# Performance work log

Measured on AMD Instinct MI355X. Metric: run time of the kernel, lower is better.

## Reference

```python
import jax, jax.numpy as jnp
import numpy as np

NL, BS, NQ, D, NH, HD, L, P, DFF, NC = 6, 16, 300, 256, 8, 32, 3, 4, 1024, 80
SHAPES = np.array([[80, 80], [40, 40], [20, 20]], np.int32)  # (H, W) per level: 640x640 input, strides 8/16/32
STARTS = np.array([0, 6400, 8000], np.int32)
LV = 8400  # sum H*W


def setup_inputs():
    keys = iter(jax.random.split(jax.random.key(0), 64))

    def rn(shape, s=0.02):
        return jax.random.normal(next(keys), shape, jnp.float32) * s

    return {
        "tgt": rn((BS, NQ, D), 1.0),
        "ref_points_unact": rn((BS, NQ, 4), 1.0),
        "memory": rn((BS, LV, D), 1.0),
        "spatial_shapes": jnp.asarray(SHAPES),
        "level_start_index": jnp.asarray(STARTS),
        "Wq": rn((NL, D, D)), "bq": rn((NL, D)),
        "Wk": rn((NL, D, D)), "bk": rn((NL, D)),
        "Wv": rn((NL, D, D)), "bv": rn((NL, D)),
        "Wo": rn((NL, D, D)), "bo": rn((NL, D)),
        "ln1_g": jnp.ones((NL, D)), "ln1_b": jnp.zeros((NL, D)),
        "ln2_g": jnp.ones((NL, D)), "ln2_b": jnp.zeros((NL, D)),
        "ln3_g": jnp.ones((NL, D)), "ln3_b": jnp.zeros((NL, D)),
        "Wvp": rn((NL, D, D)), "bvp": rn((NL, D)),
        "Woff": rn((NL, D, NH * L * P * 2)), "boff": rn((NL, NH * L * P * 2), 0.5),
        "Waw": rn((NL, D, NH * L * P)), "baw": rn((NL, NH * L * P)),
        "Wop": rn((NL, D, D)), "bop": rn((NL, D)),
        "Wff1": rn((NL, D, DFF)), "bff1": rn((NL, DFF)),
        "Wff2": rn((NL, DFF, D)), "bff2": rn((NL, D)),
        "Wb1": rn((NL, D, D)), "bb1": rn((NL, D)),
        "Wb2": rn((NL, D, D)), "bb2": rn((NL, D)),
        "Wb3": rn((NL, D, 4)), "bb3": rn((NL, 4)),
        "Ws": rn((NL, D, NC)), "bs_": rn((NL, NC)),
        "Wp1": rn((4, 2 * D)), "bp1": rn((2 * D,)),
        "Wp2": rn((2 * D, D)), "bp2": rn((D,)),
    }


def _ln(x, g, b):
    m = x.mean(-1, keepdims=True)
    v = ((x - m) ** 2).mean(-1, keepdims=True)
    return (x - m) * jax.lax.rsqrt(v + 1e-5) * g + b


def _inv_sigmoid(x, eps=1e-5):
    x = jnp.clip(x, 0.0, 1.0)
    return jnp.log(jnp.clip(x, eps, None)) - jnp.log(jnp.clip(1.0 - x, eps, None))


def _forward(shapes, starts, tgt, ref_points_unact, memory, Wq, bq, Wk, bk, Wv, bv, Wo, bo, ln1_g, ln1_b, ln2_g, ln2_b, ln3_g, ln3_b, Wvp, bvp, Woff, boff, Waw, baw, Wop, bop, Wff1, bff1, Wff2, bff2, Wb1, bb1, Wb2, bb2, Wb3, bb3, Ws, bs_, Wp1, bp1, Wp2, bp2):
    bs, Lq, _ = tgt.shape

    def mha(q, k, v, i):
        qh = (q @ Wq[i] + bq[i]).reshape(bs, Lq, NH, HD)
        kh = (k @ Wk[i] + bk[i]).reshape(bs, Lq, NH, HD)
        vh = (v @ Wv[i] + bv[i]).reshape(bs, Lq, NH, HD)
        att = jax.nn.softmax(jnp.einsum('bqhd,bkhd->bhqk', qh, kh) / np.float32(np.sqrt(HD)), -1)
        return jnp.einsum('bhqk,bkhd->bqhd', att, vh).reshape(bs, Lq, D) @ Wo[i] + bo[i]

    def deform(query, ref, i):
        # multi-scale deformable attention (Deformable-DETR core, bilinear, zero padding)
        val = (memory @ Wvp[i] + bvp[i]).reshape(bs, -1, NH, HD).transpose(0, 2, 1, 3)  # [bs,NH,Lv,HD]
        off = (query @ Woff[i] + boff[i]).reshape(bs, Lq, NH, L, P, 2)
        aw = jax.nn.softmax((query @ Waw[i] + baw[i]).reshape(bs, Lq, NH, L * P), -1).reshape(bs, Lq, NH, L, P)
        r = ref[:, :, None, None, None, :]  # [bs,Lq,1,1,1,4] box (cx,cy,w,h)
        loc = r[..., :2] + off / P * r[..., 2:] * 0.5  # [bs,Lq,NH,L,P,2]
        out = jnp.zeros((bs, NH, Lq, HD), query.dtype)
        for lvl in range(L):
            H, W = int(shapes[lvl, 0]), int(shapes[lvl, 1])
            s = int(starts[lvl])
            vl = val[:, :, s:s + H * W]  # [bs,NH,H*W,HD]
            x = loc[:, :, :, lvl, :, 0].transpose(0, 2, 1, 3) * W - 0.5  # [bs,NH,Lq,P] (align_corners=False)
            y = loc[:, :, :, lvl, :, 1].transpose(0, 2, 1, 3) * H - 0.5
            x0 = jnp.floor(x).astype(jnp.int32)
            y0 = jnp.floor(y).astype(jnp.int32)
            wx, wy = x - x0, y - y0

            def g(xi, yi):
                valid = ((xi >= 0) & (xi < W) & (yi >= 0) & (yi < H)).astype(query.dtype)
                idx = jnp.clip(yi, 0, H - 1) * W + jnp.clip(xi, 0, W - 1)
                gat = jnp.take_along_axis(vl, idx.reshape(bs, NH, Lq * P, 1), axis=2)
                return gat.reshape(bs, NH, Lq, P, HD) * valid[..., None]

            samp = (g(x0, y0) * ((1 - wx) * (1 - wy))[..., None]
                    + g(x0 + 1, y0) * (wx * (1 - wy))[..., None]
                    + g(x0, y0 + 1) * ((1 - wx) * wy)[..., None]
                    + g(x0 + 1, y0 + 1) * (wx * wy)[..., None])
            awl = aw[:, :, :, lvl].transpose(0, 2, 1, 3)  # [bs,NH,Lq,P]
            out = out + (samp * awl[..., None]).sum(3)
        return out.transpose(0, 2, 1, 3).reshape(bs, Lq, D) @ Wop[i] + bop[i]

    ref_d = jax.nn.sigmoid(ref_points_unact)
    out = tgt
    bboxes = logits = None
    for i in range(NL):
        qpos = jax.nn.relu(ref_d @ Wp1 + bp1) @ Wp2 + bp2  # query_pos_head MLP(4 -> 512 -> 256)
        q = out + qpos
        out = _ln(out + mha(q, q, out, i), ln1_g[i], ln1_b[i])
        out = _ln(out + deform(out + qpos, ref_d, i), ln2_g[i], ln2_b[i])
        out = _ln(out + jax.nn.relu(out @ Wff1[i] + bff1[i]) @ Wff2[i] + bff2[i], ln3_g[i], ln3_b[i])
        h = jax.nn.relu(out @ Wb1[i] + bb1[i])
        h = jax.nn.relu(h @ Wb2[i] + bb2[i])
        inter = jax.nn.sigmoid(h @ Wb3[i] + bb3[i] + _inv_sigmoid(ref_d))
        if i == NL - 1:  # eval_idx = -1 -> outputs taken at last layer (inference path)
            bboxes = inter[None]
            logits = (out @ Ws[i] + bs_[i])[None]
        ref_d = inter
    return bboxes, logits


def reference(tgt, ref_points_unact, memory, spatial_shapes, level_start_index, Wq, bq, Wk, bk, Wv, bv, Wo, bo, ln1_g, ln1_b, ln2_g, ln2_b, ln3_g, ln3_b, Wvp, bvp, Woff, boff, Waw, baw, Wop, bop, Wff1, bff1, Wff2, bff2, Wb1, bb1, Wb2, bb2, Wb3, bb3, Ws, bs_, Wp1, bp1, Wp2, bp2):
    shapes = np.asarray(spatial_shapes)
    starts = np.asarray(level_start_index)
    return _forward(shapes, starts, tgt, ref_points_unact, memory, Wq, bq, Wk, bk, Wv, bv, Wo, bo, ln1_g, ln1_b, ln2_g, ln2_b, ln3_g, ln3_b, Wvp, bvp, Woff, boff, Waw, baw, Wop, bop, Wff1, bff1, Wff2, bff2, Wb1, bb1, Wb2, bb2, Wb3, bb3, Ws, bs_, Wp1, bp1, Wp2, bp2)
```

## Files before the change

kernel.cpp:

```cpp
#include <hip/hip_runtime.h>

#define NLAYERS 6
#define BSZ 16
#define NQL 300
#define DM 256
#define NHEAD 8
#define HDIM 32
#define NLVL 3
#define NPT 4
#define DFFN 1024
#define NCLS 80
#define LVTOT 8400
#define NROW (BSZ * NQL)
#define MEMN (BSZ * LVTOT)

typedef __attribute__((ext_vector_type(8))) short bf16x8;
typedef __attribute__((ext_vector_type(8))) ushort us8;
typedef __attribute__((ext_vector_type(4))) float f32x4;

__device__ __forceinline__ float b2f(ushort u) {
    return __uint_as_float(((uint)u) << 16);
}
__device__ __forceinline__ ushort f2b(float f) {
    uint i = __float_as_uint(f);
    uint r = i + 0x7fffu + ((i >> 16) & 1u);
    return (ushort)(r >> 16);
}
__device__ __forceinline__ void split2(float v, ushort& h, ushort& l) {
    ushort hh = f2b(v);
    h = hh;
    l = f2b(v - b2f(hh));
}
__device__ __forceinline__ void gl_lds16(const void* g, void* l) {
    __builtin_amdgcn_global_load_lds(
        (const __attribute__((address_space(1))) unsigned int*)g,
        (__attribute__((address_space(3))) unsigned int*)l, 16, 0, 0);
}

__global__ __launch_bounds__(256) void f2b_kernel(
    const float* __restrict__ src, ushort* __restrict__ dst, int n)
{
    int i = (blockIdx.x * 256 + threadIdx.x) * 4;
    if (i < n) {
        float4 v = *(const float4*)&src[i];
        ushort4 o = {f2b(v.x), f2b(v.y), f2b(v.z), f2b(v.w)};
        *(ushort4*)&dst[i] = o;
    }
}

__global__ __launch_bounds__(256) void split_kernel(
    const float* __restrict__ src, ushort* __restrict__ dh,
    ushort* __restrict__ dl, int n)
{
    int i = (blockIdx.x * 256 + threadIdx.x) * 4;
    if (i < n) {
        float4 v = *(const float4*)&src[i];
        ushort4 h, l;
        split2(v.x, h.x, l.x);
        split2(v.y, h.y, l.y);
        split2(v.z, h.z, l.z);
        split2(v.w, h.w, l.w);
        *(ushort4*)&dh[i] = h;
        *(ushort4*)&dl[i] = l;
    }
}

#define NTE 14
struct TTab {
    const float* s[NTE];
    ushort* d[NTE];
    int K[NTE], N[NTE], dls[NTE], dr0[NTE];
    int tstart[NTE + 1];
};

__global__ __launch_bounds__(256) void transpose_batch_kernel(TTab tab)
{
    __shared__ float tile[32][33];
    const int bx = blockIdx.x;
    int e = 0;
    while (e < NTE - 1 && bx >= tab.tstart[e + 1]) ++e;
    const int local = bx - tab.tstart[e];
    const int K = tab.K[e], N = tab.N[e];
    const int tx_n = (N + 31) >> 5, ty_n = (K + 31) >> 5;
    const int perB = tx_n * ty_n;
    const int z = local / perB;
    const int rem = local - z * perB;
    const int tyi = rem / tx_n, txi = rem - tyi * tx_n;
    const float* src = tab.s[e] + (size_t)z * K * N;
    ushort* dh = tab.d[e] + (size_t)z * tab.dls[e] + (size_t)tab.dr0[e] * K;
    const int n0 = txi * 32, k0 = tyi * 32;
    const int tx = threadIdx.x, ty = threadIdx.y;
    for (int r = 0; r < 32; r += 8) {
        int k = k0 + ty + r, n = n0 + tx;
        if (k < K && n < N) tile[ty + r][tx] = src[(size_t)k * N + n];
    }
    __syncthreads();
    for (int r = 0; r < 32; r += 8) {
        int n = n0 + ty + r, k = k0 + tx;
        if (n < N && k < K) dh[(size_t)n * K + k] = f2b(tile[tx][ty + r]);
    }
}

__global__ __launch_bounds__(256) void concat2_kernel(
    const float* __restrict__ a, int na, const float* __restrict__ b, int nb,
    float* __restrict__ dst, int nl)
{
    const int tot = na + nb;
    int i = blockIdx.x * 256 + threadIdx.x;
    if (i < nl * tot) {
        int l = i / tot, j = i - l * tot;
        dst[i] = (j < na) ? a[l * na + j] : b[l * nb + j - na];
    }
}

template <int ACT>
__global__ __launch_bounds__(256) void gemm_ps(
    const ushort* __restrict__ Ahp, const ushort* __restrict__ Alp,
    const ushort* __restrict__ BTh, const float* __restrict__ bias,
    int M, int N, int K,
    float* __restrict__ Cf, const float* __restrict__ addsrc,
    ushort* __restrict__ Ch, ushort* __restrict__ Cl)
{
    __shared__ __align__(16) ushort Ahs[2][64 * 32];
    __shared__ __align__(16) ushort Als[2][64 * 32];
    __shared__ __align__(16) ushort Bhs[2][64 * 32];

    const int tid  = threadIdx.x;
    const int m0   = blockIdx.x * 64;
    const int n0   = blockIdx.y * 64;
    const int wv   = tid >> 6;
    const int lane = tid & 63;
    const int lm   = lane & 15;
    const int lq   = lane >> 4;
    const int r    = tid >> 2;
    const int c8   = (tid & 3) * 8;

    gl_lds16(&Ahp[(size_t)(m0 + r) * K + c8], &Ahs[0][r * 32 + c8]);
    gl_lds16(&Alp[(size_t)(m0 + r) * K + c8], &Als[0][r * 32 + c8]);
    gl_lds16(&BTh[(size_t)(n0 + r) * K + c8], &Bhs[0][r * 32 + c8]);
    __syncthreads();

    f32x4 acc[4] = {};
    int buf = 0;
    for (int k0 = 32; k0 < K + 32; k0 += 32) {
        const int nxt = buf ^ 1;
        if (k0 < K) {
            gl_lds16(&Ahp[(size_t)(m0 + r) * K + k0 + c8], &Ahs[nxt][r * 32 + c8]);
            gl_lds16(&Alp[(size_t)(m0 + r) * K + k0 + c8], &Als[nxt][r * 32 + c8]);
            gl_lds16(&BTh[(size_t)(n0 + r) * K + k0 + c8], &Bhs[nxt][r * 32 + c8]);
        }
        bf16x8 afh = *(const bf16x8*)&Ahs[buf][(wv * 16 + lm) * 32 + lq * 8];
        bf16x8 afl = *(const bf16x8*)&Als[buf][(wv * 16 + lm) * 32 + lq * 8];
#pragma unroll
        for (int nb = 0; nb < 4; ++nb) {
            bf16x8 bfh = *(const bf16x8*)&Bhs[buf][(nb * 16 + lm) * 32 + lq * 8];
            acc[nb] = __builtin_amdgcn_mfma_f32_16x16x32_bf16(afh, bfh, acc[nb], 0, 0, 0);
            acc[nb] = __builtin_amdgcn_mfma_f32_16x16x32_bf16(afl, bfh, acc[nb], 0, 0, 0);
        }
        __syncthreads();
        buf = nxt;
    }

    const int row = m0 + wv * 16 + lq * 4;
#pragma unroll
    for (int nb = 0; nb < 4; ++nb) {
        int col = n0 + nb * 16 + lm;
        if (col < N) {
            float bv = bias ? bias[col] : 0.f;
#pragma unroll
            for (int rr = 0; rr < 4; ++rr) {
                float v = acc[nb][rr] + bv;
                if (ACT) v = fmaxf(v, 0.f);
                const size_t idx = (size_t)(row + rr) * N + col;
                if (Cf) Cf[idx] = v;
                if (Ch) {
                    float w = addsrc ? (v + addsrc[idx]) : v;
                    ushort h, l;
                    split2(w, h, l);
                    Ch[idx] = h;
                    if (Cl) Cl[idx] = l;
                }
            }
        }
    }
}

__global__ __launch_bounds__(256) void gemm_qkv(
    const ushort* __restrict__ qhp, const ushort* __restrict__ qlp,
    const ushort* __restrict__ ohp, const ushort* __restrict__ olp,
    const ushort* __restrict__ Bqk, const ushort* __restrict__ Bv,
    const float* __restrict__ biasqk, const float* __restrict__ biasv,
    ushort* __restrict__ Cqk, ushort* __restrict__ Cv)
{
    constexpr int K = 256;
    __shared__ __align__(16) ushort Ahs[2][64 * 32];
    __shared__ __align__(16) ushort Als[2][64 * 32];
    __shared__ __align__(16) ushort Bhs[2][64 * 32];

    const int by = blockIdx.y;
    const ushort *Ahp, *Alp, *BTh;
    const float* bias;
    ushort* Ch;
    int N, n0;
    if (by < 8) { Ahp = qhp; Alp = qlp; BTh = Bqk; bias = biasqk; Ch = Cqk; N = 512; n0 = by * 64; }
    else        { Ahp = ohp; Alp = olp; BTh = Bv;  bias = biasv;  Ch = Cv;  N = 256; n0 = (by - 8) * 64; }

    const int tid  = threadIdx.x;
    const int m0   = blockIdx.x * 64;
    const int wv   = tid >> 6;
    const int lane = tid & 63;
    const int lm   = lane & 15;
    const int lq   = lane >> 4;
    const int r    = tid >> 2;
    const int c8   = (tid & 3) * 8;

    gl_lds16(&Ahp[(size_t)(m0 + r) * K + c8], &Ahs[0][r * 32 + c8]);
    gl_lds16(&Alp[(size_t)(m0 + r) * K + c8], &Als[0][r * 32 + c8]);
    gl_lds16(&BTh[(size_t)(n0 + r) * K + c8], &Bhs[0][r * 32 + c8]);
    __syncthreads();

    f32x4 acc[4] = {};
    int buf = 0;
    for (int k0 = 32; k0 < K + 32; k0 += 32) {
        const int nxt = buf ^ 1;
        if (k0 < K) {
            gl_lds16(&Ahp[(size_t)(m0 + r) * K + k0 + c8], &Ahs[nxt][r * 32 + c8]);
            gl_lds16(&Alp[(size_t)(m0 + r) * K + k0 + c8], &Als[nxt][r * 32 + c8]);
            gl_lds16(&BTh[(size_t)(n0 + r) * K + k0 + c8], &Bhs[nxt][r * 32 + c8]);
        }
        bf16x8 afh = *(const bf16x8*)&Ahs[buf][(wv * 16 + lm) * 32 + lq * 8];
        bf16x8 afl = *(const bf16x8*)&Als[buf][(wv * 16 + lm) * 32 + lq * 8];
#pragma unroll
        for (int nb = 0; nb < 4; ++nb) {
            bf16x8 bfh = *(const bf16x8*)&Bhs[buf][(nb * 16 + lm) * 32 + lq * 8];
            acc[nb] = __builtin_amdgcn_mfma_f32_16x16x32_bf16(afh, bfh, acc[nb], 0, 0, 0);
            acc[nb] = __builtin_amdgcn_mfma_f32_16x16x32_bf16(afl, bfh, acc[nb], 0, 0, 0);
        }
        __syncthreads();
        buf = nxt;
    }

    const int row = m0 + wv * 16 + lq * 4;
#pragma unroll
    for (int nb = 0; nb < 4; ++nb) {
        const int col = n0 + nb * 16 + lm;
        const float bv = bias[col];
#pragma unroll
        for (int rr = 0; rr < 4; ++rr)
            Ch[(size_t)(row + rr) * N + col] = f2b(acc[nb][rr] + bv);
    }
}

__global__ __launch_bounds__(256) void gemm_big(
    const ushort* __restrict__ Abf, const ushort* __restrict__ BTh,
    const float* __restrict__ bias, ushort* __restrict__ C,
    int M, int N, int K)
{
    __shared__ __align__(16) ushort As[128 * 32];
    __shared__ __align__(16) ushort Bs[128 * 32];
    const int tid = threadIdx.x;
    const int n0 = blockIdx.x * 128, m0 = blockIdx.y * 128;
    const int wv = tid >> 6, lane = tid & 63;
    const int lm = lane & 15, quad = lane >> 4;
    const int wr = wv >> 1, wc = wv & 1;
    const int srow = lane >> 2;
    const int scol = (lane & 3) * 8;

    f32x4 acc[4][4] = {};

    for (int k0 = 0; k0 < K; k0 += 32) {
        __syncthreads();
#pragma unroll
        for (int s2 = 0; s2 < 2; ++s2) {
            const int seg = wv * 2 + s2;
            const int row = seg * 16 + srow;
            gl_lds16(&Abf[(size_t)(m0 + row) * K + k0 + scol],
                     &As[seg * 512 + lane * 8]);
            gl_lds16(&BTh[(size_t)(n0 + row) * K + k0 + scol],
                     &Bs[seg * 512 + lane * 8]);
        }
        __syncthreads();

        bf16x8 af[4], bfr[4];
#pragma unroll
        for (int i = 0; i < 4; ++i)
            af[i] = *(const bf16x8*)&As[(wr * 64 + i * 16 + lm) * 32 + quad * 8];
#pragma unroll
        for (int i = 0; i < 4; ++i)
            bfr[i] = *(const bf16x8*)&Bs[(wc * 64 + i * 16 + lm) * 32 + quad * 8];
#pragma unroll
        for (int mi = 0; mi < 4; ++mi)
#pragma unroll
            for (int ni = 0; ni < 4; ++ni)
                acc[mi][ni] = __builtin_amdgcn_mfma_f32_16x16x32_bf16(
                    af[mi], bfr[ni], acc[mi][ni], 0, 0, 0);
    }

#pragma unroll
    for (int ni = 0; ni < 4; ++ni) {
        const int col = n0 + wc * 64 + ni * 16 + lm;
        const float bv = bias[col];
#pragma unroll
        for (int mi = 0; mi < 4; ++mi) {
            const int row = m0 + wr * 64 + mi * 16 + quad * 4;
#pragma unroll
            for (int rr = 0; rr < 4; ++rr)
                C[(size_t)(row + rr) * N + col] = f2b(acc[mi][ni][rr] + bv);
        }
    }
}

__global__ __launch_bounds__(256) void mha_mfma_kernel(
    const ushort* __restrict__ qh, int ldq, const ushort* __restrict__ kh, int ldk,
    const ushort* __restrict__ vh, int ldv,
    ushort* __restrict__ outh, ushort* __restrict__ outl)
{
    __shared__ ushort Kh[304 * 36];
    __shared__ ushort Vth[32 * 328];
    __shared__ ushort Pb[4][16 * 168];

    const int tid = threadIdx.x;
    const int wv = tid >> 6, lane = tid & 63;
    const int bh = blockIdx.x >> 1, half = blockIdx.x & 1;
    const int b = bh >> 3, h = bh & 7;
    const size_t qbase = (size_t)b * NQL * ldq + h * HDIM;
    const size_t kbase = (size_t)b * NQL * ldk + h * HDIM;
    const size_t vbase = (size_t)b * NQL * ldv + h * HDIM;
    const size_t obase = (size_t)b * NQL * DM + h * HDIM;

    for (int idx = tid; idx < 304 * 32; idx += 256) {
        int row = idx >> 5, d = idx & 31;
        Kh[row * 36 + d] = (row < NQL) ? kh[kbase + (size_t)row * ldk + d] : (ushort)0;
    }
    for (int idx = tid; idx < 328 * 32; idx += 256) {
        int key = idx >> 5, d = idx & 31;
        Vth[d * 328 + key] = (key < NQL) ? vh[vbase + (size_t)key * ldv + d] : (ushort)0;
    }
    for (int i = lane; i < 16 * 168; i += 64) Pb[wv][i] = 0;
    __syncthreads();

    const int quad = lane >> 4, c = lane & 15;
    const float scale = 0.17677669529663687f;

    const int qt_beg = (half ? 10 : 0) + wv;
    const int qt_end = (half ? 19 : 10);
    for (int qt = qt_beg; qt < qt_end; qt += 4) {
        const int q = qt * 16 + c;
        bf16x8 qf = *(const bf16x8*)&qh[qbase + (size_t)q * ldq + quad * 8];

        f32x4 sc[19];
#pragma unroll
        for (int kt = 0; kt < 19; ++kt) {
            bf16x8 kf = *(const bf16x8*)&Kh[(kt * 16 + c) * 36 + quad * 8];
            f32x4 a = {};
            a = __builtin_amdgcn_mfma_f32_16x16x32_bf16(qf, kf, a, 0, 0, 0);
            sc[kt] = a;
        }
        float inv4[4];
#pragma unroll
        for (int r = 0; r < 4; ++r) {
            float mx = -1e30f;
#pragma unroll
            for (int kt = 0; kt < 19; ++kt) {
                float s = sc[kt][r] * scale;
                if (kt * 16 + c >= NQL) s = -1e30f;
                sc[kt][r] = s;
                mx = fmaxf(mx, s);
            }
#pragma unroll
            for (int m = 1; m < 16; m <<= 1) mx = fmaxf(mx, __shfl_xor(mx, m, 64));
            float l = 0.f;
#pragma unroll
            for (int kt = 0; kt < 19; ++kt) {
                float p = __expf(sc[kt][r] - mx);
                sc[kt][r] = p;
                l += p;
            }
#pragma unroll
            for (int m = 1; m < 16; m <<= 1) l += __shfl_xor(l, m, 64);
            inv4[r] = 1.f / l;
        }

        f32x4 o0 = {}, o1 = {};
#pragma unroll
        for (int r = 0; r < 4; ++r)
#pragma unroll
            for (int kt = 0; kt < 10; ++kt)
                Pb[wv][(quad * 4 + r) * 168 + kt * 16 + c] = f2b(sc[kt][r] * inv4[r]);
#pragma unroll
        for (int ks = 0; ks < 5; ++ks) {
            bf16x8 pf = *(const bf16x8*)&Pb[wv][c * 168 + ks * 32 + quad * 8];
            bf16x8 v0 = *(const bf16x8*)&Vth[c * 328 + ks * 32 + quad * 8];
            bf16x8 v1 = *(const bf16x8*)&Vth[(16 + c) * 328 + ks * 32 + quad * 8];
            o0 = __builtin_amdgcn_mfma_f32_16x16x32_bf16(pf, v0, o0, 0, 0, 0);
            o1 = __builtin_amdgcn_mfma_f32_16x16x32_bf16(pf, v1, o1, 0, 0, 0);
        }
#pragma unroll
        for (int r = 0; r < 4; ++r) {
#pragma unroll
            for (int kt = 10; kt < 19; ++kt)
                Pb[wv][(quad * 4 + r) * 168 + (kt - 10) * 16 + c] = f2b(sc[kt][r] * inv4[r]);
            Pb[wv][(quad * 4 + r) * 168 + 144 + c] = 0;
        }
#pragma unroll
        for (int ks = 0; ks < 5; ++ks) {
            bf16x8 pf = *(const bf16x8*)&Pb[wv][c * 168 + ks * 32 + quad * 8];
            bf16x8 v0 = *(const bf16x8*)&Vth[c * 328 + 160 + ks * 32 + quad * 8];
            bf16x8 v1 = *(const bf16x8*)&Vth[(16 + c) * 328 + 160 + ks * 32 + quad * 8];
            o0 = __builtin_amdgcn_mfma_f32_16x16x32_bf16(pf, v0, o0, 0, 0, 0);
            o1 = __builtin_amdgcn_mfma_f32_16x16x32_bf16(pf, v1, o1, 0, 0, 0);
        }
#pragma unroll
        for (int r = 0; r < 4; ++r) {
            const int qq = qt * 16 + quad * 4 + r;
            if (qq < NQL) {
                ushort hh, ll;
                split2(o0[r], hh, ll);
                outh[obase + (size_t)qq * DM + c] = hh;
                outl[obase + (size_t)qq * DM + c] = ll;
                split2(o1[r], hh, ll);
                outh[obase + (size_t)qq * DM + 16 + c] = hh;
                outl[obase + (size_t)qq * DM + 16 + c] = ll;
            }
        }
    }
}

__global__ __launch_bounds__(256) void deform_kernel(
    const ushort* __restrict__ val, const float* __restrict__ offaw,
    const float* __restrict__ refd,
    ushort* __restrict__ samph, ushort* __restrict__ sampl)
{
    __shared__ float offs[192];
    __shared__ float aws[96];
    __shared__ float rr[4];
    const int row = blockIdx.x;
    const int b = row / NQL;
    const int t = threadIdx.x;
    if (t < 192) offs[t] = offaw[(size_t)row * 288 + t];
    if (t < 96)  aws[t] = offaw[(size_t)row * 288 + 192 + t];
    if (t < 4)   rr[t] = refd[row * 4 + t];
    __syncthreads();

    const int h = t >> 5, d = t & 31;
    float mx = -1e30f;
#pragma unroll
    for (int j = 0; j < 12; ++j) mx = fmaxf(mx, aws[h * 12 + j]);
    float ev[12]; float se = 0.f;
#pragma unroll
    for (int j = 0; j < 12; ++j) { ev[j] = __expf(aws[h * 12 + j] - mx); se += ev[j]; }
    const float inv = 1.f / se;

    const int HWs[3] = {80, 40, 20};
    const int STs[3] = {0, 6400, 8000};
    float acc = 0.f;
#pragma unroll
    for (int l = 0; l < NLVL; ++l) {
        const int Wd = HWs[l], Hd = HWs[l], st = STs[l];
#pragma unroll
        for (int p = 0; p < NPT; ++p) {
            const float w12 = ev[l * 4 + p] * inv;
            const float ox = offs[((h * 3 + l) * 4 + p) * 2 + 0];
            const float oy = offs[((h * 3 + l) * 4 + p) * 2 + 1];
            const float x = (rr[0] + ox * 0.125f * rr[2]) * Wd - 0.5f;
            const float y = (rr[1] + oy * 0.125f * rr[3]) * Hd - 0.5f;
            const float xf = floorf(x), yf = floorf(y);
            const int x0 = (int)xf, y0 = (int)yf;
            const float wx = x - xf, wy = y - yf;
            const float tw[4] = {(1 - wx) * (1 - wy), wx * (1 - wy),
                                 (1 - wx) * wy,       wx * wy};
            const int xs[4] = {x0, x0 + 1, x0, x0 + 1};
            const int ys[4] = {y0, y0, y0 + 1, y0 + 1};
            float sv = 0.f;
#pragma unroll
            for (int tp = 0; tp < 4; ++tp) {
                const int xi = xs[tp], yi = ys[tp];
                if (xi >= 0 && xi < Wd && yi >= 0 && yi < Hd) {
                    const int idx = st + yi * Wd + xi;
                    sv += tw[tp] * b2f(val[((size_t)b * LVTOT + idx) * DM + h * HDIM + d]);
                }
            }
            acc += w12 * sv;
        }
    }
    ushort hh, ll;
    split2(acc, hh, ll);
    samph[(size_t)row * DM + t] = hh;
    sampl[(size_t)row * DM + t] = ll;
}

__global__ __launch_bounds__(256) void addln_kernel(
    const float* x, const float* __restrict__ dl,
    const float* __restrict__ g, const float* __restrict__ bb,
    float* outf, ushort* __restrict__ outh, ushort* __restrict__ outl,
    const float* __restrict__ qpos, ushort* __restrict__ q2h, ushort* __restrict__ q2l)
{
    const int wv = threadIdx.x >> 6, lane = threadIdx.x & 63;
    const int row = blockIdx.x * 4 + wv;
    const size_t base = (size_t)row * DM + lane * 4;
    const float4 xv = *(const float4*)(x + base);
    const float4 dv = *(const float4*)(dl + base);
    float v[4] = {xv.x + dv.x, xv.y + dv.y, xv.z + dv.z, xv.w + dv.w};

    float s = v[0] + v[1] + v[2] + v[3];
#pragma unroll
    for (int m = 32; m; m >>= 1) s += __shfl_xor(s, m, 64);
    const float mean = s * (1.f / 256.f);
    float sq = 0.f;
#pragma unroll
    for (int j = 0; j < 4; ++j) { float dd = v[j] - mean; sq += dd * dd; }
#pragma unroll
    for (int m = 32; m; m >>= 1) sq += __shfl_xor(sq, m, 64);
    const float rstd = rsqrtf(sq * (1.f / 256.f) + 1e-5f);

    float y[4];
    ushort4 yh, yl;
#pragma unroll
    for (int j = 0; j < 4; ++j) {
        const int col = lane * 4 + j;
        y[j] = (v[j] - mean) * rstd * g[col] + bb[col];
    }
    *(float4*)(outf + base) = make_float4(y[0], y[1], y[2], y[3]);
    split2(y[0], yh.x, yl.x);
    split2(y[1], yh.y, yl.y);
    split2(y[2], yh.z, yl.z);
    split2(y[3], yh.w, yl.w);
    *(ushort4*)(outh + base) = yh;
    *(ushort4*)(outl + base) = yl;
    if (q2h) {
        const float4 qp = *(const float4*)(qpos + base);
        float q2v[4] = {y[0] + qp.x, y[1] + qp.y, y[2] + qp.z, y[3] + qp.w};
        ushort4 qh_, ql_;
        split2(q2v[0], qh_.x, ql_.x);
        split2(q2v[1], qh_.y, ql_.y);
        split2(q2v[2], qh_.z, ql_.z);
        split2(q2v[3], qh_.w, ql_.w);
        *(ushort4*)(q2h + base) = qh_;
        *(ushort4*)(q2l + base) = ql_;
    }
}

__global__ __launch_bounds__(256) void bbox_fused(
    const ushort* __restrict__ h2h, const ushort* __restrict__ h2l,
    const float* __restrict__ Wb3, const float* __restrict__ bb3,
    const float* __restrict__ rpu, float* __restrict__ refd,
    float* __restrict__ dout, int mode, int writeout,
    const float* __restrict__ Wp1, const float* __restrict__ bp1,
    ushort* __restrict__ t1h, ushort* __restrict__ t1l, int computeT1)
{
    __shared__ float hls[64 * 258];
    __shared__ float wb3s[1024];
    __shared__ float wp1s[4 * 512];
    __shared__ float bp1s[512];
    __shared__ float ref4[64 * 4];

    const int tid = threadIdx.x;
    const int r0 = blockIdx.x * 64;

    if (computeT1) {
        for (int i = tid; i < 2048; i += 256) wp1s[i] = Wp1[i];
        if (tid < 256) { bp1s[tid] = bp1[tid]; bp1s[tid + 256] = bp1[tid + 256]; }
    }
    if (mode == 1) {
        for (int i = tid; i < 1024; i += 256) wb3s[i] = Wb3[i];
        for (int j = tid; j < 2048; j += 256) {
            const int row = j >> 5, seg = (j & 31) * 8;
            const size_t g = (size_t)(r0 + row) * 256 + seg;
            us8 hv = *(const us8*)&h2h[g];
            us8 lv = *(const us8*)&h2l[g];
            float* o = &hls[row * 258 + seg];
#pragma unroll
            for (int x = 0; x < 8; ++x) o[x] = b2f(hv[x]) + b2f(lv[x]);
        }
    }
    __syncthreads();

    const int r = tid >> 2, c = tid & 3;
    float v;
    if (mode == 1) {
        float acc = 0.f;
        const float* hrow = &hls[r * 258];
#pragma unroll 4
        for (int k = 0; k < 256; ++k)
            acc = fmaf(hrow[k], wb3s[k * 4 + c], acc);
        const float b3v = acc + bb3[c];
        const float old = refd[(size_t)(r0 + r) * 4 + c];
        const float rc = fminf(fmaxf(old, 0.f), 1.f);
        const float invs = logf(fmaxf(rc, 1e-5f)) - logf(fmaxf(1.f - rc, 1e-5f));
        v = 1.f / (1.f + __expf(-(b3v + invs)));
    } else {
        v = 1.f / (1.f + __expf(-rpu[(size_t)(r0 + r) * 4 + c]));
    }
    refd[(size_t)(r0 + r) * 4 + c] = v;
    if (writeout) dout[(size_t)(r0 + r) * 4 + c] = v;
    ref4[r * 4 + c] = v;
    __syncthreads();

    if (!computeT1) return;
    for (int j = 0; j < 128; ++j) {
        const int idx = j * 256 + tid;
        const int row = idx >> 9, n = idx & 511;
        const float a0 = ref4[row * 4 + 0], a1 = ref4[row * 4 + 1];
        const float a2 = ref4[row * 4 + 2], a3 = ref4[row * 4 + 3];
        float t = bp1s[n];
        t = fmaf(a0, wp1s[n], t);
        t = fmaf(a1, wp1s[512 + n], t);
        t = fmaf(a2, wp1s[1024 + n], t);
        t = fmaf(a3, wp1s[1536 + n], t);
        t = fmaxf(t, 0.f);
        ushort hh, ll;
        split2(t, hh, ll);
        const size_t gg = (size_t)(r0 + row) * 512 + n;
        t1h[gg] = hh;
        t1l[gg] = ll;
    }
}

extern "C" void kernel_launch(void* const* d_in, const int* in_sizes, int n_in,
                              void* d_out, int out_size, void* d_ws, size_t ws_size,
                              hipStream_t stream)
{
    const float* tgt    = (const float*)d_in[0];
    const float* rpu    = (const float*)d_in[1];
    const float* memory = (const float*)d_in[2];
    const float* Wq  = (const float*)d_in[5];  const float* bq  = (const float*)d_in[6];
    const float* Wk  = (const float*)d_in[7];  const float* bk  = (const float*)d_in[8];
    const float* Wv  = (const float*)d_in[9];  const float* bv  = (const float*)d_in[10];
    const float* Wo  = (const float*)d_in[11]; const float* bo  = (const float*)d_in[12];
    const float* ln1g = (const float*)d_in[13]; const float* ln1b = (const float*)d_in[14];
    const float* ln2g = (const float*)d_in[15]; const float* ln2b = (const float*)d_in[16];
    const float* ln3g = (const float*)d_in[17]; const float* ln3b = (const float*)d_in[18];
    const float* Wvp = (const float*)d_in[19]; const float* bvp = (const float*)d_in[20];
    const float* Woff = (const float*)d_in[21]; const float* boff = (const float*)d_in[22];
    const float* Waw = (const float*)d_in[23]; const float* baw = (const float*)d_in[24];
    const float* Wop = (const float*)d_in[25]; const float* bop = (const float*)d_in[26];
    const float* Wff1 = (const float*)d_in[27]; const float* bff1 = (const float*)d_in[28];
    const float* Wff2 = (const float*)d_in[29]; const float* bff2 = (const float*)d_in[30];
    const float* Wb1 = (const float*)d_in[31]; const float* bb1 = (const float*)d_in[32];
    const float* Wb2 = (const float*)d_in[33]; const float* bb2 = (const float*)d_in[34];
    const float* Wb3 = (const float*)d_in[35]; const float* bb3 = (const float*)d_in[36];
    const float* Ws  = (const float*)d_in[37]; const float* bs_ = (const float*)d_in[38];
    const float* Wp1 = (const float*)d_in[39]; const float* bp1 = (const float*)d_in[40];
    const float* Wp2 = (const float*)d_in[41]; const float* bp2 = (const float*)d_in[42];

    size_t off = 0;
    auto alloc = [&](size_t elems, size_t elsz) -> void* {
        void* r = (char*)d_ws + off;
        off += elems * elsz;
        off = (off + 255) & ~(size_t)255;
        return r;
    };
    ushort *wqkh = (ushort*)alloc(6 * 131072, 2);
    ushort *wvh  = (ushort*)alloc(6 * 65536, 2);
    ushort *woh  = (ushort*)alloc(6 * 65536, 2);
    ushort *wvph = (ushort*)alloc(6 * 65536, 2);
    ushort *wfah = (ushort*)alloc(6 * 81920, 2);
    ushort *woph = (ushort*)alloc(6 * 65536, 2);
    ushort *wf1h = (ushort*)alloc(6 * 262144, 2);
    ushort *wf2h = (ushort*)alloc(6 * 262144, 2);
    ushort *wb1h = (ushort*)alloc(6 * 65536, 2);
    ushort *wb2h = (ushort*)alloc(6 * 65536, 2);
    ushort *wsh  = (ushort*)alloc(6 * 20480, 2);
    ushort *wp2h = (ushort*)alloc(131072, 2);
    float  *bqk  = (float*)alloc(6 * 512, 4);
    float  *bfa  = (float*)alloc(6 * 288, 4);

    ushort* mem_bf = (ushort*)alloc((size_t)MEMN * DM, 2);
    ushort* val_bf = (ushort*)alloc((size_t)MEMN * DM, 2);
    float*  out_f  = (float*)alloc(NROW * DM, 4);
    float*  qpos_f = (float*)alloc(NROW * DM, 4);
    float*  tmp_f  = (float*)alloc(NROW * DM, 4);
    float*  refd_f = (float*)alloc(NROW * 4, 4);
    float*  offaw_f = (float*)alloc(NROW * 288, 4);

    ushort* out_h = (ushort*)alloc(NROW * DM, 2);
    ushort* out_l = (ushort*)alloc(NROW * DM, 2);

    const size_t NN = NROW;
    ushort* scratch = (ushort*)alloc(NN * 2056, 2);
    ushort* q_h  = scratch;
    ushort* q_l  = scratch + NN * 256;
    ushort* vh_h = scratch + NN * 512;
    ushort* att_h = scratch;
    ushort* att_l = scratch + NN * 256;
    ushort* q2_h = scratch + NN * 512;
    ushort* q2_l = scratch + NN * 768;
    ushort* samp_h = scratch;
    ushort* samp_l = scratch + NN * 256;
    ushort* ff_h = scratch;
    ushort* ff_l = scratch + NN * 1024;
    ushort* h1_h = scratch;
    ushort* h1_l = scratch + NN * 256;
    ushort* h2_h = scratch + NN * 512;
    ushort* h2_l = scratch + NN * 768;
    ushort* t1_h = scratch + NN * 1024;
    ushort* t1_l = scratch + NN * 1536;
    ushort* qk_h = scratch + NN * 1024;

    if (off > ws_size) return;

    {
        TTab tab;
        const float* ss[NTE] = {Wq, Wk, Wv, Wo, Wvp, Woff, Waw, Wop,
                                Wff1, Wff2, Wb1, Wb2, Ws, Wp2};
        ushort* dd[NTE] = {wqkh, wqkh, wvh, woh, wvph, wfah, wfah, woph,
                           wf1h, wf2h, wb1h, wb2h, wsh, wp2h};
        const int KK[NTE]  = {256, 256, 256, 256, 256, 256, 256, 256,
                              256, 1024, 256, 256, 256, 512};
        const int NNe[NTE] = {256, 256, 256, 256, 256, 192, 96, 256,
                              1024, 256, 256, 256, 80, 256};
        const int BB[NTE]  = {6, 6, 6, 6, 6, 6, 6, 6, 6, 6, 6, 6, 6, 1};
        const int DL[NTE]  = {131072, 131072, 65536, 65536, 65536, 81920, 81920,
                              65536, 262144, 262144, 65536, 65536, 20480, 131072};
        const int DR[NTE]  = {0, 256, 0, 0, 0, 0, 192, 0, 0, 0, 0, 0, 0, 0};
        int total = 0;
        for (int e = 0; e < NTE; ++e) {
            tab.s[e] = ss[e]; tab.d[e] = dd[e];
            tab.K[e] = KK[e]; tab.N[e] = NNe[e];
            tab.dls[e] = DL[e]; tab.dr0[e] = DR[e];
            tab.tstart[e] = total;
            total += ((NNe[e] + 31) / 32) * ((KK[e] + 31) / 32) * BB[e];
        }
        tab.tstart[NTE] = total;
        transpose_batch_kernel<<<total, dim3(32, 8), 0, stream>>>(tab);
    }
    concat2_kernel<<<12, 256, 0, stream>>>(bq, 256, bk, 256, bqk, 6);
    concat2_kernel<<<7, 256, 0, stream>>>(boff, 192, baw, 96, bfa, 6);
    f2b_kernel<<<(MEMN * DM) / 1024, 256, 0, stream>>>(memory, mem_bf, MEMN * DM);

    hipMemcpyAsync(out_f, tgt, (size_t)NROW * DM * 4, hipMemcpyDeviceToDevice, stream);
    split_kernel<<<(NROW * DM) / 1024, 256, 0, stream>>>(tgt, out_h, out_l, NROW * DM);
    bbox_fused<<<75, 256, 0, stream>>>(nullptr, nullptr, Wb3, bb3, rpu, refd_f,
                                       nullptr, 0, 0, Wp1, bp1, t1_h, t1_l, 1);

    auto GP = [&](const ushort* Ahp, const ushort* Alp, const ushort* BTh,
                  const float* bias, int N, int K, bool relu,
                  float* Cf, ushort* Ch = nullptr, ushort* Cl = nullptr,
                  const float* addsrc = nullptr) {
        dim3 g(NROW / 64, (N + 63) / 64);
        if (relu) gemm_ps<1><<<g, 256, 0, stream>>>(Ahp, Alp, BTh, bias, NROW, N, K,
                                                    Cf, addsrc, Ch, Cl);
        else      gemm_ps<0><<<g, 256, 0, stream>>>(Ahp, Alp, BTh, bias, NROW, N, K,
                                                    Cf, addsrc, Ch, Cl);
    };

    for (int i = 0; i < NLAYERS; ++i) {
        GP(t1_h, t1_l, wp2h, bp2, 256, 512, false, qpos_f, q_h, q_l, out_f);
        gemm_qkv<<<dim3(NROW / 64, 12), 256, 0, stream>>>(
            q_h, q_l, out_h, out_l, wqkh + i * 131072, wvh + i * 65536,
            bqk + i * 512, bv + i * 256, qk_h, vh_h);
        mha_mfma_kernel<<<256, 256, 0, stream>>>(qk_h, 512, qk_h + 256, 512,
                                                 vh_h, 256, att_h, att_l);
        GP(att_h, att_l, woh + i * 65536, bo + i * 256, 256, 256, false, tmp_f);
        addln_kernel<<<1200, 256, 0, stream>>>(out_f, tmp_f, ln1g + i * 256, ln1b + i * 256,
                                               out_f, out_h, out_l, qpos_f, q2_h, q2_l);
        {
            dim3 g(DM / 128, MEMN / 128);
            gemm_big<<<g, 256, 0, stream>>>(mem_bf, wvph + i * 65536, bvp + i * 256,
                                            val_bf, MEMN, DM, DM);
        }
        GP(q2_h, q2_l, wfah + i * 81920, bfa + i * 288, 288, 256, false, offaw_f);
        deform_kernel<<<4800, 256, 0, stream>>>(val_bf, offaw_f, refd_f, samp_h, samp_l);
        GP(samp_h, samp_l, woph + i * 65536, bop + i * 256, 256, 256, false, tmp_f);
        addln_kernel<<<1200, 256, 0, stream>>>(out_f, tmp_f, ln2g + i * 256, ln2b + i * 256,
                                               out_f, out_h, out_l, nullptr, nullptr, nullptr);
        GP(out_h, out_l, wf1h + i * 262144, bff1 + i * 1024, 1024, 256, true,
           nullptr, ff_h, ff_l);
        GP(ff_h, ff_l, wf2h + i * 262144, bff2 + i * 256, 256, 1024, false, tmp_f);
        addln_kernel<<<1200, 256, 0, stream>>>(out_f, tmp_f, ln3g + i * 256, ln3b + i * 256,
                                               out_f, out_h, out_l, nullptr, nullptr, nullptr);
        GP(out_h, out_l, wb1h + i * 65536, bb1 + i * 256, 256, 256, true,
           nullptr, h1_h, h1_l);
        GP(h1_h, h1_l, wb2h + i * 65536, bb2 + i * 256, 256, 256, true,
           nullptr, h2_h, h2_l);
        const int last = (i == NLAYERS - 1);
        bbox_fused<<<75, 256, 0, stream>>>(h2_h, h2_l, Wb3 + i * 1024, bb3 + i * 4,
                                           nullptr, refd_f, (float*)d_out, 1,
                                           last ? 1 : 0, Wp1, bp1, t1_h, t1_l,
                                           last ? 0 : 1);
        if (last) {
            GP(out_h, out_l, wsh + i * 20480, bs_ + i * 80, 80, 256, false,
               (float*)d_out + NROW * 4);
        }
    }
}
```

Before: 2.105 ms.

## Split value-projection GEMM into chunks co-scheduled with small layer GEMMs

Removes the standalone memory value-projection GEMM and splits its 2100 tiles into three 700-tile chunks. Each chunk runs as extra blocks inside a combined kernel alongside one of the small per-layer GEMMs (query-pos, output projection, offset/attention-weight projection). The aim is to fill the GPU's idle compute units during the under-occupied small GEMMs and to cut launches. It also merges the two bias-concat kernels into one and vectorizes the t1 stores in bbox_fused to 8-wide writes. The cost is a larger LDS footprint for the small-GEMM blocks and more complex kernels.

Result: no change. 2.097 ms (-0.4%).

```diff
diff --git a/kernel.cpp b/kernel.cpp
--- a/kernel.cpp
+++ b/kernel.cpp
@@ -101,15 +101,23 @@
     }
 }
 
-__global__ __launch_bounds__(256) void concat2_kernel(
-    const float* __restrict__ a, int na, const float* __restrict__ b, int nb,
-    float* __restrict__ dst, int nl)
-{
-    const int tot = na + nb;
-    int i = blockIdx.x * 256 + threadIdx.x;
-    if (i < nl * tot) {
-        int l = i / tot, j = i - l * tot;
-        dst[i] = (j < na) ? a[l * na + j] : b[l * nb + j - na];
+__global__ __launch_bounds__(256) void concat_both_kernel(
+    const float* __restrict__ bq, const float* __restrict__ bk, float* __restrict__ bqk,
+    const float* __restrict__ boff, const float* __restrict__ baw, float* __restrict__ bfa)
+{
+    const int bx = blockIdx.x;
+    if (bx < 12) {
+        int i = bx * 256 + threadIdx.x;
+        if (i < 6 * 512) {
+            int l = i / 512, j = i - l * 512;
+            bqk[i] = (j < 256) ? bq[l * 256 + j] : bk[l * 256 + j - 256];
+        }
+    } else {
+        int i = (bx - 12) * 256 + threadIdx.x;
+        if (i < 6 * 288) {
+            int l = i / 288, j = i - l * 288;
+            bfa[i] = (j < 192) ? boff[l * 192 + j] : baw[l * 96 + j - 192];
+        }
     }
 }
 
@@ -185,6 +193,137 @@
     }
 }
 
+__global__ __launch_bounds__(256) void gemm_mix(
+    const ushort* __restrict__ Ahp, const ushort* __restrict__ Alp,
+    const ushort* __restrict__ BTh, const float* __restrict__ bias,
+    int N, int K,
+    float* __restrict__ Cf, const float* __restrict__ addsrc,
+    ushort* __restrict__ Ch, ushort* __restrict__ Cl,
+    int nSmall,
+    const ushort* __restrict__ gA, const ushort* __restrict__ gB,
+    const float* __restrict__ gbias, ushort* __restrict__ gC,
+    int chunkOff)
+{
+    __shared__ __align__(16) ushort lds[12288];
+
+    const int tid  = threadIdx.x;
+    const int wv   = tid >> 6;
+    const int lane = tid & 63;
+    const int lm   = lane & 15;
+    const int lq   = lane >> 4;
+
+    if ((int)blockIdx.x < nSmall) {
+        typedef ushort (*lds2)[64 * 32];
+        lds2 Ahs = (lds2)lds;
+        lds2 Als = (lds2)(lds + 4096);
+        lds2 Bhs = (lds2)(lds + 8192);
+        const int m0 = (blockIdx.x % 75) * 64;
+        const int n0 = (blockIdx.x / 75) * 64;
+        const int r  = tid >> 2;
+        const int c8 = (tid & 3) * 8;
+
+        gl_lds16(&Ahp[(size_t)(m0 + r) * K + c8], &Ahs[0][r * 32 + c8]);
+        gl_lds16(&Alp[(size_t)(m0 + r) * K + c8], &Als[0][r * 32 + c8]);
+        gl_lds16(&BTh[(size_t)(n0 + r) * K + c8], &Bhs[0][r * 32 + c8]);
+        __syncthreads();
+
+        f32x4 acc[4] = {};
+        int buf = 0;
+        for (int k0 = 32; k0 < K + 32; k0 += 32) {
+            const int nxt = buf ^ 1;
+            if (k0 < K) {
+                gl_lds16(&Ahp[(size_t)(m0 + r) * K + k0 + c8], &Ahs[nxt][r * 32 + c8]);
+                gl_lds16(&Alp[(size_t)(m0 + r) * K + k0 + c8], &Als[nxt][r * 32 + c8]);
+                gl_lds16(&BTh[(size_t)(n0 + r) * K + k0 + c8], &Bhs[nxt][r * 32 + c8]);
+            }
+            bf16x8 afh = *(const bf16x8*)&Ahs[buf][(wv * 16 + lm) * 32 + lq * 8];
+            bf16x8 afl = *(const bf16x8*)&Als[buf][(wv * 16 + lm) * 32 + lq * 8];
+#pragma unroll
+            for (int nb = 0; nb < 4; ++nb) {
+                bf16x8 bfh = *(const bf16x8*)&Bhs[buf][(nb * 16 + lm) * 32 + lq * 8];
+                acc[nb] = __builtin_amdgcn_mfma_f32_16x16x32_bf16(afh, bfh, acc[nb], 0, 0, 0);
+                acc[nb] = __builtin_amdgcn_mfma_f32_16x16x32_bf16(afl, bfh, acc[nb], 0, 0, 0);
+            }
+            __syncthreads();
+            buf = nxt;
+        }
+
+        const int row = m0 + wv * 16 + lq * 4;
+#pragma unroll
+        for (int nb = 0; nb < 4; ++nb) {
+            int col = n0 + nb * 16 + lm;
+            if (col < N) {
+                float bv = bias[col];
+#pragma unroll
+                for (int rr = 0; rr < 4; ++rr) {
+                    float v = acc[nb][rr] + bv;
+                    const size_t idx = (size_t)(row + rr) * N + col;
+                    if (Cf) Cf[idx] = v;
+                    if (Ch) {
+                        float w = addsrc ? (v + addsrc[idx]) : v;
+                        ushort h, l;
+                        split2(w, h, l);
+                        Ch[idx] = h;
+                        if (Cl) Cl[idx] = l;
+                    }
+                }
+            }
+        }
+    } else {
+        ushort* As = lds;
+        ushort* Bs = lds + 4096;
+        const int bid = (int)blockIdx.x - nSmall + chunkOff;
+        const int n0 = (bid & 1) * 128;
+        const int m0 = (bid >> 1) * 128;
+        const int wr = wv >> 1, wc = wv & 1;
+        const int srow = lane >> 2;
+        const int scol = (lane & 3) * 8;
+
+        f32x4 acc[4][4] = {};
+
+        for (int k0 = 0; k0 < 256; k0 += 32) {
+            __syncthreads();
+#pragma unroll
+            for (int s2 = 0; s2 < 2; ++s2) {
+                const int seg = wv * 2 + s2;
+                const int row = seg * 16 + srow;
+                gl_lds16(&gA[(size_t)(m0 + row) * 256 + k0 + scol],
+                         &As[seg * 512 + lane * 8]);
+                gl_lds16(&gB[(size_t)(n0 + row) * 256 + k0 + scol],
+                         &Bs[seg * 512 + lane * 8]);
+            }
+            __syncthreads();
+
+            bf16x8 af[4], bfr[4];
+#pragma unroll
+            for (int i = 0; i < 4; ++i)
+                af[i] = *(const bf16x8*)&As[(wr * 64 + i * 16 + lm) * 32 + lq * 8];
+#pragma unroll
+            for (int i = 0; i < 4; ++i)
+                bfr[i] = *(const bf16x8*)&Bs[(wc * 64 + i * 16 + lm) * 32 + lq * 8];
+#pragma unroll
+            for (int mi = 0; mi < 4; ++mi)
+#pragma unroll
+                for (int ni = 0; ni < 4; ++ni)
+                    acc[mi][ni] = __builtin_amdgcn_mfma_f32_16x16x32_bf16(
+                        af[mi], bfr[ni], acc[mi][ni], 0, 0, 0);
+        }
+
+#pragma unroll
+        for (int ni = 0; ni < 4; ++ni) {
+            const int col = n0 + wc * 64 + ni * 16 + lm;
+            const float bv = gbias[col];
+#pragma unroll
+            for (int mi = 0; mi < 4; ++mi) {
+                const int row = m0 + wr * 64 + mi * 16 + lq * 4;
+#pragma unroll
+                for (int rr = 0; rr < 4; ++rr)
+                    gC[(size_t)(row + rr) * 256 + col] = f2b(acc[mi][ni][rr] + bv);
+            }
+        }
+    }
+}
+
 __global__ __launch_bounds__(256) void gemm_qkv(
     const ushort* __restrict__ qhp, const ushort* __restrict__ qlp,
     const ushort* __restrict__ ohp, const ushort* __restrict__ olp,
@@ -248,65 +387,6 @@
 #pragma unroll
         for (int rr = 0; rr < 4; ++rr)
             Ch[(size_t)(row + rr) * N + col] = f2b(acc[nb][rr] + bv);
-    }
-}
-
-__global__ __launch_bounds__(256) void gemm_big(
-    const ushort* __restrict__ Abf, const ushort* __restrict__ BTh,
-    const float* __restrict__ bias, ushort* __restrict__ C,
-    int M, int N, int K)
-{
-    __shared__ __align__(16) ushort As[128 * 32];
-    __shared__ __align__(16) ushort Bs[128 * 32];
-    const int tid = threadIdx.x;
-    const int n0 = blockIdx.x * 128, m0 = blockIdx.y * 128;
-    const int wv = tid >> 6, lane = tid & 63;
-    const int lm = lane & 15, quad = lane >> 4;
-    const int wr = wv >> 1, wc = wv & 1;
-    const int srow = lane >> 2;
-    const int scol = (lane & 3) * 8;
-
-    f32x4 acc[4][4] = {};
-
-    for (int k0 = 0; k0 < K; k0 += 32) {
-        __syncthreads();
-#pragma unroll
-        for (int s2 = 0; s2 < 2; ++s2) {
-            const int seg = wv * 2 + s2;
-            const int row = seg * 16 + srow;
-            gl_lds16(&Abf[(size_t)(m0 + row) * K + k0 + scol],
-                     &As[seg * 512 + lane * 8]);
-            gl_lds16(&BTh[(size_t)(n0 + row) * K + k0 + scol],
-                     &Bs[seg * 512 + lane * 8]);
-        }
-        __syncthreads();
-
-        bf16x8 af[4], bfr[4];
-#pragma unroll
-        for (int i = 0; i < 4; ++i)
-            af[i] = *(const bf16x8*)&As[(wr * 64 + i * 16 + lm) * 32 + quad * 8];
-#pragma unroll
-        for (int i = 0; i < 4; ++i)
-            bfr[i] = *(const bf16x8*)&Bs[(wc * 64 + i * 16 + lm) * 32 + quad * 8];
-#pragma unroll
-        for (int mi = 0; mi < 4; ++mi)
-#pragma unroll
-            for (int ni = 0; ni < 4; ++ni)
-                acc[mi][ni] = __builtin_amdgcn_mfma_f32_16x16x32_bf16(
-                    af[mi], bfr[ni], acc[mi][ni], 0, 0, 0);
-    }
-
-#pragma unroll
-    for (int ni = 0; ni < 4; ++ni) {
-        const int col = n0 + wc * 64 + ni * 16 + lm;
-        const float bv = bias[col];
-#pragma unroll
-        for (int mi = 0; mi < 4; ++mi) {
-            const int row = m0 + wr * 64 + mi * 16 + quad * 4;
-#pragma unroll
-            for (int rr = 0; rr < 4; ++rr)
-                C[(size_t)(row + rr) * N + col] = f2b(acc[mi][ni][rr] + bv);
-        }
     }
 }
 
@@ -597,22 +677,29 @@
     __syncthreads();
 
     if (!computeT1) return;
-    for (int j = 0; j < 128; ++j) {
-        const int idx = j * 256 + tid;
-        const int row = idx >> 9, n = idx & 511;
+#pragma unroll
+    for (int jj = 0; jj < 16; ++jj) {
+        const int idx = jj * 2048 + tid * 8;
+        const int row = idx >> 9, nb = idx & 511;
         const float a0 = ref4[row * 4 + 0], a1 = ref4[row * 4 + 1];
         const float a2 = ref4[row * 4 + 2], a3 = ref4[row * 4 + 3];
-        float t = bp1s[n];
-        t = fmaf(a0, wp1s[n], t);
-        t = fmaf(a1, wp1s[512 + n], t);
-        t = fmaf(a2, wp1s[1024 + n], t);
-        t = fmaf(a3, wp1s[1536 + n], t);
-        t = fmaxf(t, 0.f);
-        ushort hh, ll;
-        split2(t, hh, ll);
-        const size_t gg = (size_t)(r0 + row) * 512 + n;
-        t1h[gg] = hh;
-        t1l[gg] = ll;
+        us8 hv, lv;
+#pragma unroll
+        for (int x = 0; x < 8; ++x) {
+            const int n = nb + x;
+            float t = bp1s[n];
+            t = fmaf(a0, wp1s[n], t);
+            t = fmaf(a1, wp1s[512 + n], t);
+            t = fmaf(a2, wp1s[1024 + n], t);
+            t = fmaf(a3, wp1s[1536 + n], t);
+            t = fmaxf(t, 0.f);
+            ushort hh, ll;
+            split2(t, hh, ll);
+            hv[x] = hh; lv[x] = ll;
+        }
+        const size_t gg = (size_t)(r0 + row) * 512 + nb;
+        *(us8*)&t1h[gg] = hv;
+        *(us8*)&t1l[gg] = lv;
     }
 }
 
@@ -724,8 +811,7 @@
         tab.tstart[NTE] = total;
         transpose_batch_kernel<<<total, dim3(32, 8), 0, stream>>>(tab);
     }
-    concat2_kernel<<<12, 256, 0, stream>>>(bq, 256, bk, 256, bqk, 6);
-    concat2_kernel<<<7, 256, 0, stream>>>(boff, 192, baw, 96, bfa, 6);
+    concat_both_kernel<<<19, 256, 0, stream>>>(bq, bk, bqk, boff, baw, bfa);
     f2b_kernel<<<(MEMN * DM) / 1024, 256, 0, stream>>>(memory, mem_bf, MEMN * DM);
 
     hipMemcpyAsync(out_f, tgt, (size_t)NROW * DM * 4, hipMemcpyDeviceToDevice, stream);
@@ -745,21 +831,26 @@
     };
 
     for (int i = 0; i < NLAYERS; ++i) {
-        GP(t1_h, t1_l, wp2h, bp2, 256, 512, false, qpos_f, q_h, q_l, out_f);
+        const ushort* wvp_i = wvph + i * 65536;
+        const float*  bvp_i = bvp + i * 256;
+        gemm_mix<<<300 + 700, 256, 0, stream>>>(
+            t1_h, t1_l, wp2h, bp2, 256, 512, qpos_f, out_f, q_h, q_l,
+            300, mem_bf, wvp_i, bvp_i, val_bf, 0);
         gemm_qkv<<<dim3(NROW / 64, 12), 256, 0, stream>>>(
             q_h, q_l, out_h, out_l, wqkh + i * 131072, wvh + i * 65536,
             bqk + i * 512, bv + i * 256, qk_h, vh_h);
         mha_mfma_kernel<<<256, 256, 0, stream>>>(qk_h, 512, qk_h + 256, 512,
                                                  vh_h, 256, att_h, att_l);
-        GP(att_h, att_l, woh + i * 65536, bo + i * 256, 256, 256, false, tmp_f);
+        gemm_mix<<<300 + 700, 256, 0, stream>>>(
+            att_h, att_l, woh + i * 65536, bo + i * 256, 256, 256, tmp_f,
+            nullptr, nullptr, nullptr,
+            300, mem_bf, wvp_i, bvp_i, val_bf, 700);
         addln_kernel<<<1200, 256, 0, stream>>>(out_f, tmp_f, ln1g + i * 256, ln1b + i * 256,
                                                out_f, out_h, out_l, qpos_f, q2_h, q2_l);
-        {
-            dim3 g(DM / 128, MEMN / 128);
-            gemm_big<<<g, 256, 0, stream>>>(mem_bf, wvph + i * 65536, bvp + i * 256,
-                                            val_bf, MEMN, DM, DM);
-        }
-        GP(q2_h, q2_l, wfah + i * 81920, bfa + i * 288, 288, 256, false, offaw_f);
+        gemm_mix<<<375 + 700, 256, 0, stream>>>(
+            q2_h, q2_l, wfah + i * 81920, bfa + i * 288, 288, 256, offaw_f,
+            nullptr, nullptr, nullptr,
+            375, mem_bf, wvp_i, bvp_i, val_bf, 1400);
         deform_kernel<<<4800, 256, 0, stream>>>(val_bf, offaw_f, refd_f, samp_h, samp_l);
         GP(samp_h, samp_l, woph + i * 65536, bop + i * 256, 256, 256, false, tmp_f);
         addln_kernel<<<1200, 256, 0, stream>>>(out_f, tmp_f, ln2g + i * 256, ln2b + i * 256,
```
